# Performance work log

Hardware: AMD Instinct MI355X
Metric: run time of the kernel (lower is better)

Reference implementation:

```python
import jax, jax.numpy as jnp
import numpy as np

N = 50000
NFEAT = 256
NHID = 64
NHEADS = 8
E_RAND = 1600000
ALPHA = 0.2  # leaky relu negative slope


def setup_inputs() -> dict:
    key = jax.random.key(0)
    kx, ke1, ke2, kw, ka, kwo, kao = jax.random.split(key, 7)
    x = jax.random.normal(kx, (N, NFEAT), dtype=jnp.float32)
    src = jax.random.randint(ke1, (E_RAND,), 0, N)
    dst = jax.random.randint(ke2, (E_RAND,), 0, N)
    loops = jnp.arange(N)
    edge_index = jnp.stack([jnp.concatenate([src, loops]),
                            jnp.concatenate([dst, loops])], axis=0)  # [2, 1650000]
    # learned params (xavier-ish scale)
    W = jax.random.normal(kw, (NHEADS, NFEAT, NHID), dtype=jnp.float32) * (1.0 / np.sqrt(NFEAT))
    a = jax.random.normal(ka, (NHEADS, 2 * NHID), dtype=jnp.float32) * (1.0 / np.sqrt(2 * NHID))
    W_out = jax.random.normal(kwo, (NHID * NHEADS, 1), dtype=jnp.float32) * (1.0 / np.sqrt(NHID * NHEADS))
    a_out = jax.random.normal(kao, (2,), dtype=jnp.float32) * (1.0 / np.sqrt(2.0))
    return {"x": x, "edge_index": edge_index, "W": W, "a": a,
            "W_out": W_out, "a_out": a_out}


def _sp_gat_layer(x, edge_index, W_l, a_l, concat):
    """pyGAT SpGraphAttentionLayer forward (eval mode: dropout = identity)."""
    src, dst = edge_index[0], edge_index[1]
    h = x @ W_l                              # [N, F']
    F_ = h.shape[1]
    # a^T [h_src || h_dst] = (a1.h)[src] + (a2.h)[dst] -- avoids [2F', E] concat
    f1 = h @ a_l[:F_]                        # [N]
    f2 = h @ a_l[F_:]                        # [N]
    s = f1[src] + f2[dst]                    # [E]
    e = jnp.exp(-jax.nn.leaky_relu(s, ALPHA))  # [E], note the minus sign (pyGAT)
    rowsum = jax.ops.segment_sum(e, src, num_segments=N)          # [N]
    num = jax.ops.segment_sum(e[:, None] * h[dst], src, num_segments=N)  # [N, F']
    out = num / rowsum[:, None]
    return jax.nn.elu(out) if concat else out


def reference(x, edge_index, W, a, W_out, a_out):
    # input dropout is identity in eval mode
    heads = [_sp_gat_layer(x, edge_index, W[i], a[i], concat=True)
             for i in range(NHEADS)]
    h = jnp.concatenate(heads, axis=1)       # [N, NHEADS*NHID]
    out = _sp_gat_layer(h, edge_index, W_out, a_out, concat=False)  # [N, 1]
    return jax.nn.sigmoid(jax.nn.elu(out))
```

## Files before the change

kernel.cpp:

```cpp
#include <hip/hip_runtime.h>
#include <hip/hip_bf16.h>
#include <hip/hip_fp16.h>
#include <math.h>

#define N_NODES 50000
#define NFEAT 256
#define NHID 64
#define NHEADS 8
#define FTOT 512
#define E_TOT 1650000
#define ALPHA 0.2f
#define NB_SCAN 196
#define ALDS 264
#define GEMM_BLKS 782
#define SCAT_BLKS 3223
#define LOG2E 1.442695040888963f

typedef short s16x4 __attribute__((ext_vector_type(4)));
typedef short s16x8 __attribute__((ext_vector_type(8)));
typedef float f32x4 __attribute__((ext_vector_type(4)));
typedef float f32x2 __attribute__((ext_vector_type(2)));

__device__ __forceinline__ short f2bf(float f) {
  unsigned u = __float_as_uint(f);
  unsigned r = u + 0x7fffu + ((u >> 16) & 1u);
  return (short)(r >> 16);
}

__device__ __forceinline__ unsigned char f2fp8(float f) {
  return (unsigned char)(__builtin_amdgcn_cvt_pk_fp8_f32(f, 0.f, 0, false) & 0xff);
}

__device__ __forceinline__ float att_e(float f1v, float g) {
  float s = f1v + g;
  float lk = fmaxf(s, ALPHA * s);
  return __builtin_amdgcn_exp2f(-LOG2E * lk);
}

__device__ __forceinline__ void fma8_fp8(float e, uint2 u, f32x2* acc2) {
  f32x2 ev; ev[0] = e; ev[1] = e;
  acc2[0] += ev * __builtin_amdgcn_cvt_pk_f32_fp8(u.x, false);
  acc2[1] += ev * __builtin_amdgcn_cvt_pk_f32_fp8(u.x, true);
  acc2[2] += ev * __builtin_amdgcn_cvt_pk_f32_fp8(u.y, false);
  acc2[3] += ev * __builtin_amdgcn_cvt_pk_f32_fp8(u.y, true);
}

__global__ __launch_bounds__(256) void setup_kernel(
    const float* __restrict__ W, short* __restrict__ Wt,
    const int* __restrict__ src, int* __restrict__ cnt,
    int* __restrict__ rank) {
  int b = blockIdx.x, t = threadIdx.x;
  if (b < 512) {
    int idx = b * 256 + t;
    int h = idx >> 14, r = idx & 16383, k = r >> 6, j = r & 63;
    Wt[h * 16384 + j * 256 + k] = f2bf(W[idx]);
  } else {
    int i = (b - 512) * 256 + t;
    if (i < E_TOT) rank[i] = atomicAdd(&cnt[src[i]], 1);
  }
}

__global__ __launch_bounds__(256) void scan1_kernel(const int* __restrict__ cnt,
                                                    int* __restrict__ offs,
                                                    int* __restrict__ bsum) {
  __shared__ int sh[256];
  int b = blockIdx.x, t = threadIdx.x, i = b * 256 + t;
  int v = (i < N_NODES) ? cnt[i] : 0;
  sh[t] = v;
  __syncthreads();
  for (int o = 1; o < 256; o <<= 1) {
    int u = (t >= o) ? sh[t - o] : 0;
    __syncthreads();
    sh[t] += u;
    __syncthreads();
  }
  if (i < N_NODES) offs[i] = sh[t] - v;
  if (t == 255) bsum[b] = sh[255];
}

__global__ __launch_bounds__(256) void scan2_kernel(int* __restrict__ bsum,
                                                    int* __restrict__ offs) {
  __shared__ int sh[256];
  int t = threadIdx.x;
  int v = (t < NB_SCAN) ? bsum[t] : 0;
  sh[t] = v;
  __syncthreads();
  for (int o = 1; o < 256; o <<= 1) {
    int u = (t >= o) ? sh[t - o] : 0;
    __syncthreads();
    sh[t] += u;
    __syncthreads();
  }
  if (t < NB_SCAN) bsum[t] = sh[t] - v;
  if (t == 255) offs[N_NODES] = sh[255];
}

__global__ __launch_bounds__(256) void scan3_kernel(int* __restrict__ offs,
                                                    const int* __restrict__ bsum) {
  int i = blockIdx.x * 256 + threadIdx.x;
  if (i < N_NODES) offs[i] += bsum[blockIdx.x];
}

__global__ __launch_bounds__(512) void gemm_scatter_kernel(
    const float* __restrict__ x, const short* __restrict__ Wt,
    const float* __restrict__ a, unsigned char* __restrict__ h1,
    float* __restrict__ f1, float* __restrict__ f2,
    const int* __restrict__ src, const int* __restrict__ dst,
    const int* __restrict__ offsets, const int* __restrict__ rank,
    int* __restrict__ edst) {
  if (blockIdx.x >= GEMM_BLKS) {
    int i = (blockIdx.x - GEMM_BLKS) * 512 + threadIdx.x;
    if (i < E_TOT) edst[offsets[src[i]] + rank[i]] = dst[i];
    return;
  }
  __shared__ __align__(16) short A_s[64 * ALDS];
  int bm = blockIdx.x * 64;
  int t = threadIdx.x;
  int wid = t >> 6, l = t & 63;
  int lr = l & 15, lk = l >> 4;
  int arow = t >> 3, acol = (t & 7) * 4;
  const short* wbase = Wt + wid * 16384 + lr * 256 + lk * 8;
  int gr = bm + arow;
  float4 xr[8];
#pragma unroll
  for (int i = 0; i < 8; ++i) {
    if (gr < N_NODES)
      xr[i] = *reinterpret_cast<const float4*>(x + (size_t)gr * NFEAT + i * 32 + acol);
    else
      xr[i] = make_float4(0.f, 0.f, 0.f, 0.f);
  }
#pragma unroll
  for (int i = 0; i < 8; ++i) {
    s16x4 v;
    v[0] = f2bf(xr[i].x); v[1] = f2bf(xr[i].y);
    v[2] = f2bf(xr[i].z); v[3] = f2bf(xr[i].w);
    *reinterpret_cast<s16x4*>(&A_s[arow * ALDS + i * 32 + acol]) = v;
  }
  __syncthreads();
  f32x4 acc[4][4] = {};
  for (int k0 = 0; k0 < NFEAT; k0 += 32) {
    s16x8 bf[4];
#pragma unroll
    for (int nj = 0; nj < 4; ++nj)
      bf[nj] = *reinterpret_cast<const s16x8*>(wbase + nj * 16 * 256 + k0);
    s16x8 af[4];
#pragma unroll
    for (int mi = 0; mi < 4; ++mi)
      af[mi] = *reinterpret_cast<const s16x8*>(
          &A_s[(mi * 16 + lr) * ALDS + k0 + lk * 8]);
#pragma unroll
    for (int mi = 0; mi < 4; ++mi)
#pragma unroll
      for (int nj = 0; nj < 4; ++nj)
        acc[mi][nj] = __builtin_amdgcn_mfma_f32_16x16x32_bf16(
            af[mi], bf[nj], acc[mi][nj], 0, 0, 0);
  }
#pragma unroll
  for (int mi = 0; mi < 4; ++mi) {
#pragma unroll
    for (int nj = 0; nj < 4; ++nj) {
#pragma unroll
      for (int q = 0; q < 4; ++q) {
        int r = bm + mi * 16 + lk * 4 + q;
        if (r < N_NODES)
          h1[(size_t)r * FTOT + wid * 64 + nj * 16 + lr] = f2fp8(acc[mi][nj][q]);
      }
    }
  }
  float a1v[4], a2v[4];
#pragma unroll
  for (int nj = 0; nj < 4; ++nj) {
    a1v[nj] = a[wid * 128 + nj * 16 + lr];
    a2v[nj] = a[wid * 128 + 64 + nj * 16 + lr];
  }
#pragma unroll
  for (int mi = 0; mi < 4; ++mi) {
#pragma unroll
    for (int q = 0; q < 4; ++q) {
      float p1 = 0.f, p2 = 0.f;
#pragma unroll
      for (int nj = 0; nj < 4; ++nj) {
        p1 += acc[mi][nj][q] * a1v[nj];
        p2 += acc[mi][nj][q] * a2v[nj];
      }
      p1 += __shfl_xor(p1, 1); p2 += __shfl_xor(p2, 1);
      p1 += __shfl_xor(p1, 2); p2 += __shfl_xor(p2, 2);
      p1 += __shfl_xor(p1, 4); p2 += __shfl_xor(p2, 4);
      p1 += __shfl_xor(p1, 8); p2 += __shfl_xor(p2, 8);
      int r = bm + mi * 16 + lk * 4 + q;
      if (lr == 0 && r < N_NODES) {
        f1[r * 8 + wid] = p1;
        f2[r * 8 + wid] = p2;
      }
    }
  }
}

__global__ __launch_bounds__(256) void aggregate_kernel(
    const unsigned char* __restrict__ h1, const float* __restrict__ f1,
    const float* __restrict__ f2, const int* __restrict__ offsets,
    const int* __restrict__ edst, const float* __restrict__ W_out,
    float* __restrict__ hout) {
  int wv = __builtin_amdgcn_readfirstlane(threadIdx.x >> 6);
  int n = blockIdx.x * 4 + wv;
  int l = threadIdx.x & 63;
  int head = l >> 3;
  int beg = offsets[n], end = offsets[n + 1];
  float f1v = f1[n * 8 + head];
  f32x2 acc2[4] = {};
  float rs = 0.f;
  int j = beg;
  for (; j + 3 < end; j += 4) {
    int d0 = edst[j], d1 = edst[j + 1], d2 = edst[j + 2], d3 = edst[j + 3];
    uint2 u0 = *reinterpret_cast<const uint2*>(h1 + (size_t)d0 * FTOT + l * 8);
    uint2 u1 = *reinterpret_cast<const uint2*>(h1 + (size_t)d1 * FTOT + l * 8);
    uint2 u2 = *reinterpret_cast<const uint2*>(h1 + (size_t)d2 * FTOT + l * 8);
    uint2 u3 = *reinterpret_cast<const uint2*>(h1 + (size_t)d3 * FTOT + l * 8);
    float g0 = f2[d0 * 8 + head];
    float g1 = f2[d1 * 8 + head];
    float g2 = f2[d2 * 8 + head];
    float g3 = f2[d3 * 8 + head];
    float e0 = att_e(f1v, g0), e1 = att_e(f1v, g1);
    float e2 = att_e(f1v, g2), e3 = att_e(f1v, g3);
    rs += (e0 + e1) + (e2 + e3);
    fma8_fp8(e0, u0, acc2);
    fma8_fp8(e1, u1, acc2);
    fma8_fp8(e2, u2, acc2);
    fma8_fp8(e3, u3, acc2);
  }
  for (; j < end; ++j) {
    int d = edst[j];
    uint2 u = *reinterpret_cast<const uint2*>(h1 + (size_t)d * FTOT + l * 8);
    float e = att_e(f1v, f2[d * 8 + head]);
    rs += e;
    fma8_fp8(e, u, acc2);
  }
  float inv = 1.f / rs;
  float v = 0.f;
  const float* wop = W_out + l * 8;
#pragma unroll
  for (int k = 0; k < 4; ++k) {
#pragma unroll
    for (int q = 0; q < 2; ++q) {
      float o = acc2[k][q] * inv;
      o = (o > 0.f) ? o : expm1f(o);
      v += o * wop[k * 2 + q];
    }
  }
#pragma unroll
  for (int o = 32; o > 0; o >>= 1) v += __shfl_down(v, o);
  if (l == 0) hout[n] = v;
}

__global__ __launch_bounds__(256) void layer2_kernel(
    const int* __restrict__ offsets, const int* __restrict__ edst,
    const float* __restrict__ hout, const float* __restrict__ a_out,
    float* __restrict__ out) {
  int wv = __builtin_amdgcn_readfirstlane(threadIdx.x >> 6);
  int n = blockIdx.x * 4 + wv;
  int l = threadIdx.x & 63;
  float a0 = a_out[0], a1 = a_out[1];
  int beg = offsets[n], end = offsets[n + 1];
  float f1v = hout[n] * a0;
  float rs = 0.f, num = 0.f;
  for (int j = beg + l; j < end; j += 64) {
    int d = edst[j];
    float hd = hout[d];
    float s = f1v + a1 * hd;
    float lk = fmaxf(s, ALPHA * s);
    float e = __builtin_amdgcn_exp2f(-LOG2E * lk);
    rs += e;
    num += e * hd;
  }
#pragma unroll
  for (int o = 32; o > 0; o >>= 1) {
    rs += __shfl_down(rs, o);
    num += __shfl_down(num, o);
  }
  if (l == 0) {
    float o_ = num / rs;
    float el = (o_ > 0.f) ? o_ : expm1f(o_);
    out[n] = 1.f / (1.f + __builtin_amdgcn_exp2f(-LOG2E * el));
  }
}

extern "C" void kernel_launch(void* const* d_in, const int* in_sizes, int n_in,
                              void* d_out, int out_size, void* d_ws, size_t ws_size,
                              hipStream_t stream) {
  const float* x = (const float*)d_in[0];
  const int* ei = (const int*)d_in[1];
  const float* W = (const float*)d_in[2];
  const float* a = (const float*)d_in[3];
  const float* W_out = (const float*)d_in[4];
  const float* a_out = (const float*)d_in[5];
  float* out = (float*)d_out;
  const int* src = ei;
  const int* dst = ei + E_TOT;

  char* p = (char*)d_ws;
  auto carve = [&](size_t bytes) {
    char* r = p;
    p += (bytes + 255) & ~(size_t)255;
    return r;
  };
  unsigned char* h1 = (unsigned char*)carve((size_t)N_NODES * FTOT);
  float* f1 = (float*)carve((size_t)N_NODES * 8 * 4);
  float* f2 = (float*)carve((size_t)N_NODES * 8 * 4);
  int* offsets = (int*)carve((size_t)(N_NODES + 1) * 4);
  int* cnt = (int*)carve((size_t)N_NODES * 4);
  int* rank = (int*)carve((size_t)E_TOT * 4);
  int* edst = (int*)carve((size_t)E_TOT * 4);
  int* bsum = (int*)carve((size_t)NB_SCAN * 4);
  short* Wt = (short*)carve((size_t)NHEADS * NFEAT * NHID * 2);
  float* hout = (float*)carve((size_t)N_NODES * 4);

  hipMemsetAsync(cnt, 0, (size_t)N_NODES * 4, stream);

  setup_kernel<<<512 + 6446, 256, 0, stream>>>(W, Wt, src, cnt, rank);
  scan1_kernel<<<NB_SCAN, 256, 0, stream>>>(cnt, offsets, bsum);
  scan2_kernel<<<1, 256, 0, stream>>>(bsum, offsets);
  scan3_kernel<<<NB_SCAN, 256, 0, stream>>>(offsets, bsum);
  gemm_scatter_kernel<<<GEMM_BLKS + SCAT_BLKS, 512, 0, stream>>>(
      x, Wt, a, h1, f1, f2, src, dst, offsets, rank, edst);
  aggregate_kernel<<<12500, 256, 0, stream>>>(h1, f1, f2, offsets, edst, W_out, hout);
  layer2_kernel<<<12500, 256, 0, stream>>>(offsets, edst, hout, a_out, out);
}
```

Before: 291.7 us.

## Bucket CSR edges by destination range for gather locality; fuse scan passes

Builds the CSR with a compound key (src, dst>>12), so each source's neighbor list is partially sorted into 13 destination tiles. The intent is better cache locality for the gathers of h1 rows and f2 values in the aggregate kernel. The scan becomes a 16-elements-per-thread two-kernel scan over 650k keys, with scan2 and scan3 merged. The -log2e factor is folded into f1/f2 at GEMM time to remove a multiply per edge. In exchange, the count, offset and scan arrays are 13x larger and cost more memory traffic.

```diff
diff --git a/kernel.cpp b/kernel.cpp
--- a/kernel.cpp
+++ b/kernel.cpp
@@ -10,12 +10,16 @@
 #define FTOT 512
 #define E_TOT 1650000
 #define ALPHA 0.2f
-#define NB_SCAN 196
 #define ALDS 264
 #define GEMM_BLKS 782
 #define SCAT_BLKS 3223
 #define LOG2E 1.442695040888963f
 
+#define NT 13
+#define NK (N_NODES * NT)
+#define SC_ELEMS 4096
+#define NB1 159
+
 typedef short s16x4 __attribute__((ext_vector_type(4)));
 typedef short s16x8 __attribute__((ext_vector_type(8)));
 typedef float f32x4 __attribute__((ext_vector_type(4)));
@@ -29,12 +33,6 @@
 
 __device__ __forceinline__ unsigned char f2fp8(float f) {
   return (unsigned char)(__builtin_amdgcn_cvt_pk_fp8_f32(f, 0.f, 0, false) & 0xff);
-}
-
-__device__ __forceinline__ float att_e(float f1v, float g) {
-  float s = f1v + g;
-  float lk = fmaxf(s, ALPHA * s);
-  return __builtin_amdgcn_exp2f(-LOG2E * lk);
 }
 
 __device__ __forceinline__ void fma8_fp8(float e, uint2 u, f32x2* acc2) {
@@ -47,8 +45,8 @@
 
 __global__ __launch_bounds__(256) void setup_kernel(
     const float* __restrict__ W, short* __restrict__ Wt,
-    const int* __restrict__ src, int* __restrict__ cnt,
-    int* __restrict__ rank) {
+    const int* __restrict__ src, const int* __restrict__ dst,
+    int* __restrict__ cnt, int* __restrict__ rank) {
   int b = blockIdx.x, t = threadIdx.x;
   if (b < 512) {
     int idx = b * 256 + t;
@@ -56,7 +54,10 @@
     Wt[h * 16384 + j * 256 + k] = f2bf(W[idx]);
   } else {
     int i = (b - 512) * 256 + t;
-    if (i < E_TOT) rank[i] = atomicAdd(&cnt[src[i]], 1);
+    if (i < E_TOT) {
+      int key = src[i] * NT + (dst[i] >> 12);
+      rank[i] = atomicAdd(&cnt[key], 1);
+    }
   }
 }
 
@@ -64,8 +65,46 @@
                                                     int* __restrict__ offs,
                                                     int* __restrict__ bsum) {
   __shared__ int sh[256];
-  int b = blockIdx.x, t = threadIdx.x, i = b * 256 + t;
-  int v = (i < N_NODES) ? cnt[i] : 0;
+  int b = blockIdx.x, t = threadIdx.x;
+  int base = b * SC_ELEMS + t * 16;
+  int v[16];
+  int s = 0;
+  if (base < NK) {
+#pragma unroll
+    for (int k = 0; k < 4; ++k) {
+      int4 q = *reinterpret_cast<const int4*>(cnt + base + k * 4);
+      v[4 * k] = q.x; v[4 * k + 1] = q.y; v[4 * k + 2] = q.z; v[4 * k + 3] = q.w;
+    }
+#pragma unroll
+    for (int k = 0; k < 16; ++k) s += v[k];
+  } else {
+#pragma unroll
+    for (int k = 0; k < 16; ++k) v[k] = 0;
+  }
+  sh[t] = s;
+  __syncthreads();
+  for (int o = 1; o < 256; o <<= 1) {
+    int u = (t >= o) ? sh[t - o] : 0;
+    __syncthreads();
+    sh[t] += u;
+    __syncthreads();
+  }
+  int run = sh[t] - s;
+  if (base < NK) {
+#pragma unroll
+    for (int k = 0; k < 16; ++k) {
+      offs[base + k] = run;
+      run += v[k];
+    }
+  }
+  if (t == 255) bsum[b] = sh[255];
+}
+
+__global__ __launch_bounds__(256) void scan23_kernel(
+    const int* __restrict__ bsum, int* __restrict__ offs) {
+  __shared__ int sh[256];
+  int b = blockIdx.x, t = threadIdx.x;
+  int v = (t < NB1) ? bsum[t] : 0;
   sh[t] = v;
   __syncthreads();
   for (int o = 1; o < 256; o <<= 1) {
@@ -74,31 +113,13 @@
     sh[t] += u;
     __syncthreads();
   }
-  if (i < N_NODES) offs[i] = sh[t] - v;
-  if (t == 255) bsum[b] = sh[255];
-}
-
-__global__ __launch_bounds__(256) void scan2_kernel(int* __restrict__ bsum,
-                                                    int* __restrict__ offs) {
-  __shared__ int sh[256];
-  int t = threadIdx.x;
-  int v = (t < NB_SCAN) ? bsum[t] : 0;
-  sh[t] = v;
-  __syncthreads();
-  for (int o = 1; o < 256; o <<= 1) {
-    int u = (t >= o) ? sh[t - o] : 0;
-    __syncthreads();
-    sh[t] += u;
-    __syncthreads();
-  }
-  if (t < NB_SCAN) bsum[t] = sh[t] - v;
-  if (t == 255) offs[N_NODES] = sh[255];
-}
-
-__global__ __launch_bounds__(256) void scan3_kernel(int* __restrict__ offs,
-                                                    const int* __restrict__ bsum) {
-  int i = blockIdx.x * 256 + threadIdx.x;
-  if (i < N_NODES) offs[i] += bsum[blockIdx.x];
+  int base = (b > 0) ? sh[b - 1] : 0;
+  int i0 = b * SC_ELEMS + t * 16;
+  if (i0 < NK) {
+#pragma unroll
+    for (int k = 0; k < 16; ++k) offs[i0 + k] += base;
+  }
+  if (b == 0 && t == 0) offs[NK] = sh[NB1 - 1];
 }
 
 __global__ __launch_bounds__(512) void gemm_scatter_kernel(
@@ -110,7 +131,11 @@
     int* __restrict__ edst) {
   if (blockIdx.x >= GEMM_BLKS) {
     int i = (blockIdx.x - GEMM_BLKS) * 512 + threadIdx.x;
-    if (i < E_TOT) edst[offsets[src[i]] + rank[i]] = dst[i];
+    if (i < E_TOT) {
+      int d = dst[i];
+      int key = src[i] * NT + (d >> 12);
+      edst[offsets[key] + rank[i]] = d;
+    }
     return;
   }
   __shared__ __align__(16) short A_s[64 * ALDS];
@@ -189,8 +214,8 @@
       p1 += __shfl_xor(p1, 8); p2 += __shfl_xor(p2, 8);
       int r = bm + mi * 16 + lk * 4 + q;
       if (lr == 0 && r < N_NODES) {
-        f1[r * 8 + wid] = p1;
-        f2[r * 8 + wid] = p2;
+        f1[r * 8 + wid] = -LOG2E * p1;
+        f2[r * 8 + wid] = -LOG2E * p2;
       }
     }
   }
@@ -205,8 +230,8 @@
   int n = blockIdx.x * 4 + wv;
   int l = threadIdx.x & 63;
   int head = l >> 3;
-  int beg = offsets[n], end = offsets[n + 1];
-  float f1v = f1[n * 8 + head];
+  int beg = offsets[n * NT], end = offsets[n * NT + NT];
+  float F = f1[n * 8 + head];
   f32x2 acc2[4] = {};
   float rs = 0.f;
   int j = beg;
@@ -220,8 +245,11 @@
     float g1 = f2[d1 * 8 + head];
     float g2 = f2[d2 * 8 + head];
     float g3 = f2[d3 * 8 + head];
-    float e0 = att_e(f1v, g0), e1 = att_e(f1v, g1);
-    float e2 = att_e(f1v, g2), e3 = att_e(f1v, g3);
+    float c0 = F + g0, c1 = F + g1, c2 = F + g2, c3 = F + g3;
+    float e0 = __builtin_amdgcn_exp2f(fminf(c0, ALPHA * c0));
+    float e1 = __builtin_amdgcn_exp2f(fminf(c1, ALPHA * c1));
+    float e2 = __builtin_amdgcn_exp2f(fminf(c2, ALPHA * c2));
+    float e3 = __builtin_amdgcn_exp2f(fminf(c3, ALPHA * c3));
     rs += (e0 + e1) + (e2 + e3);
     fma8_fp8(e0, u0, acc2);
     fma8_fp8(e1, u1, acc2);
@@ -231,7 +259,8 @@
   for (; j < end; ++j) {
     int d = edst[j];
     uint2 u = *reinterpret_cast<const uint2*>(h1 + (size_t)d * FTOT + l * 8);
-    float e = att_e(f1v, f2[d * 8 + head]);
+    float cs = F + f2[d * 8 + head];
+    float e = __builtin_amdgcn_exp2f(fminf(cs, ALPHA * cs));
     rs += e;
     fma8_fp8(e, u, acc2);
   }
@@ -260,7 +289,7 @@
   int n = blockIdx.x * 4 + wv;
   int l = threadIdx.x & 63;
   float a0 = a_out[0], a1 = a_out[1];
-  int beg = offsets[n], end = offsets[n + 1];
+  int beg = offsets[n * NT], end = offsets[n * NT + NT];
   float f1v = hout[n] * a0;
   float rs = 0.f, num = 0.f;
   for (int j = beg + l; j < end; j += 64) {
@@ -306,20 +335,19 @@
   unsigned char* h1 = (unsigned char*)carve((size_t)N_NODES * FTOT);
   float* f1 = (float*)carve((size_t)N_NODES * 8 * 4);
   float* f2 = (float*)carve((size_t)N_NODES * 8 * 4);
-  int* offsets = (int*)carve((size_t)(N_NODES + 1) * 4);
-  int* cnt = (int*)carve((size_t)N_NODES * 4);
+  int* offsets = (int*)carve((size_t)(NK + 1) * 4);
+  int* cnt = (int*)carve((size_t)NK * 4);
   int* rank = (int*)carve((size_t)E_TOT * 4);
   int* edst = (int*)carve((size_t)E_TOT * 4);
-  int* bsum = (int*)carve((size_t)NB_SCAN * 4);
+  int* bsum = (int*)carve((size_t)NB1 * 4);
   short* Wt = (short*)carve((size_t)NHEADS * NFEAT * NHID * 2);
   float* hout = (float*)carve((size_t)N_NODES * 4);
 
-  hipMemsetAsync(cnt, 0, (size_t)N_NODES * 4, stream);
-
-  setup_kernel<<<512 + 6446, 256, 0, stream>>>(W, Wt, src, cnt, rank);
-  scan1_kernel<<<NB_SCAN, 256, 0, stream>>>(cnt, offsets, bsum);
-  scan2_kernel<<<1, 256, 0, stream>>>(bsum, offsets);
-  scan3_kernel<<<NB_SCAN, 256, 0, stream>>>(offsets, bsum);
+  hipMemsetAsync(cnt, 0, (size_t)NK * 4, stream);
+
+  setup_kernel<<<512 + 6446, 256, 0, stream>>>(W, Wt, src, dst, cnt, rank);
+  scan1_kernel<<<NB1, 256, 0, stream>>>(cnt, offsets, bsum);
+  scan23_kernel<<<NB1, 256, 0, stream>>>(bsum, offsets);
   gemm_scatter_kernel<<<GEMM_BLKS + SCAT_BLKS, 512, 0, stream>>>(
       x, Wt, a, h1, f1, f2, src, dst, offsets, rank, edst);
   aggregate_kernel<<<12500, 256, 0, stream>>>(h1, f1, f2, offsets, edst, W_out, hout);
```

New measurement: 297.3 us. No clear change (+1.9%).

## Fuse atomic histogram with GEMM, merge scan passes, prescale attention logits

Applied to the files above, without the earlier changes.

Moves the per-edge atomic degree histogram out of the setup kernel and co-schedules it with the GEMM blocks. The scatter now runs as its own kernel after the scan. The memset is replaced by zeroing cnt inside the weight-conversion kernel. Scan stages 2 and 3 are merged, so every block redundantly scans the block sums. f1/f2 are pre-multiplied by -log2e so the aggregate loop does one fmin plus exp2 instead of fmax, multiply and exp2. The aim is fewer launches and overlapping the atomic-bound histogram with the compute-bound GEMM. In exchange the scatter loses its overlap with the GEMM.

```diff
diff --git a/kernel.cpp b/kernel.cpp
--- a/kernel.cpp
+++ b/kernel.cpp
@@ -13,7 +13,7 @@
 #define NB_SCAN 196
 #define ALDS 264
 #define GEMM_BLKS 782
-#define SCAT_BLKS 3223
+#define HIST_BLKS 3223
 #define LOG2E 1.442695040888963f
 
 typedef short s16x4 __attribute__((ext_vector_type(4)));
@@ -29,12 +29,6 @@
 
 __device__ __forceinline__ unsigned char f2fp8(float f) {
   return (unsigned char)(__builtin_amdgcn_cvt_pk_fp8_f32(f, 0.f, 0, false) & 0xff);
-}
-
-__device__ __forceinline__ float att_e(float f1v, float g) {
-  float s = f1v + g;
-  float lk = fmaxf(s, ALPHA * s);
-  return __builtin_amdgcn_exp2f(-LOG2E * lk);
 }
 
 __device__ __forceinline__ void fma8_fp8(float e, uint2 u, f32x2* acc2) {
@@ -45,10 +39,8 @@
   acc2[3] += ev * __builtin_amdgcn_cvt_pk_f32_fp8(u.y, true);
 }
 
-__global__ __launch_bounds__(256) void setup_kernel(
-    const float* __restrict__ W, short* __restrict__ Wt,
-    const int* __restrict__ src, int* __restrict__ cnt,
-    int* __restrict__ rank) {
+__global__ __launch_bounds__(256) void wconv_zero_kernel(
+    const float* __restrict__ W, short* __restrict__ Wt, int* __restrict__ cnt) {
   int b = blockIdx.x, t = threadIdx.x;
   if (b < 512) {
     int idx = b * 256 + t;
@@ -56,7 +48,101 @@
     Wt[h * 16384 + j * 256 + k] = f2bf(W[idx]);
   } else {
     int i = (b - 512) * 256 + t;
+    if (i < N_NODES) cnt[i] = 0;
+  }
+}
+
+__global__ __launch_bounds__(512) void gemm_hist_kernel(
+    const float* __restrict__ x, const short* __restrict__ Wt,
+    const float* __restrict__ a, unsigned char* __restrict__ h1,
+    float* __restrict__ f1, float* __restrict__ f2,
+    const int* __restrict__ src, int* __restrict__ cnt,
+    int* __restrict__ rank) {
+  if (blockIdx.x >= GEMM_BLKS) {
+    int i = (blockIdx.x - GEMM_BLKS) * 512 + threadIdx.x;
     if (i < E_TOT) rank[i] = atomicAdd(&cnt[src[i]], 1);
+    return;
+  }
+  __shared__ __align__(16) short A_s[64 * ALDS];
+  int bm = blockIdx.x * 64;
+  int t = threadIdx.x;
+  int wid = t >> 6, l = t & 63;
+  int lr = l & 15, lk = l >> 4;
+  int arow = t >> 3, acol = (t & 7) * 4;
+  const short* wbase = Wt + wid * 16384 + lr * 256 + lk * 8;
+  int gr = bm + arow;
+  float4 xr[8];
+#pragma unroll
+  for (int i = 0; i < 8; ++i) {
+    if (gr < N_NODES)
+      xr[i] = *reinterpret_cast<const float4*>(x + (size_t)gr * NFEAT + i * 32 + acol);
+    else
+      xr[i] = make_float4(0.f, 0.f, 0.f, 0.f);
+  }
+#pragma unroll
+  for (int i = 0; i < 8; ++i) {
+    s16x4 v;
+    v[0] = f2bf(xr[i].x); v[1] = f2bf(xr[i].y);
+    v[2] = f2bf(xr[i].z); v[3] = f2bf(xr[i].w);
+    *reinterpret_cast<s16x4*>(&A_s[arow * ALDS + i * 32 + acol]) = v;
+  }
+  __syncthreads();
+  f32x4 acc[4][4] = {};
+  for (int k0 = 0; k0 < NFEAT; k0 += 32) {
+    s16x8 bf[4];
+#pragma unroll
+    for (int nj = 0; nj < 4; ++nj)
+      bf[nj] = *reinterpret_cast<const s16x8*>(wbase + nj * 16 * 256 + k0);
+    s16x8 af[4];
+#pragma unroll
+    for (int mi = 0; mi < 4; ++mi)
+      af[mi] = *reinterpret_cast<const s16x8*>(
+          &A_s[(mi * 16 + lr) * ALDS + k0 + lk * 8]);
+#pragma unroll
+    for (int mi = 0; mi < 4; ++mi)
+#pragma unroll
+      for (int nj = 0; nj < 4; ++nj)
+        acc[mi][nj] = __builtin_amdgcn_mfma_f32_16x16x32_bf16(
+            af[mi], bf[nj], acc[mi][nj], 0, 0, 0);
+  }
+#pragma unroll
+  for (int mi = 0; mi < 4; ++mi) {
+#pragma unroll
+    for (int nj = 0; nj < 4; ++nj) {
+#pragma unroll
+      for (int q = 0; q < 4; ++q) {
+        int r = bm + mi * 16 + lk * 4 + q;
+        if (r < N_NODES)
+          h1[(size_t)r * FTOT + wid * 64 + nj * 16 + lr] = f2fp8(acc[mi][nj][q]);
+      }
+    }
+  }
+  float a1v[4], a2v[4];
+#pragma unroll
+  for (int nj = 0; nj < 4; ++nj) {
+    a1v[nj] = a[wid * 128 + nj * 16 + lr];
+    a2v[nj] = a[wid * 128 + 64 + nj * 16 + lr];
+  }
+#pragma unroll
+  for (int mi = 0; mi < 4; ++mi) {
+#pragma unroll
+    for (int q = 0; q < 4; ++q) {
+      float p1 = 0.f, p2 = 0.f;
+#pragma unroll
+      for (int nj = 0; nj < 4; ++nj) {
+        p1 += acc[mi][nj][q] * a1v[nj];
+        p2 += acc[mi][nj][q] * a2v[nj];
+      }
+      p1 += __shfl_xor(p1, 1); p2 += __shfl_xor(p2, 1);
+      p1 += __shfl_xor(p1, 2); p2 += __shfl_xor(p2, 2);
+      p1 += __shfl_xor(p1, 4); p2 += __shfl_xor(p2, 4);
+      p1 += __shfl_xor(p1, 8); p2 += __shfl_xor(p2, 8);
+      int r = bm + mi * 16 + lk * 4 + q;
+      if (lr == 0 && r < N_NODES) {
+        f1[r * 8 + wid] = -LOG2E * p1;
+        f2[r * 8 + wid] = -LOG2E * p2;
+      }
+    }
   }
 }
 
@@ -78,10 +164,10 @@
   if (t == 255) bsum[b] = sh[255];
 }
 
-__global__ __launch_bounds__(256) void scan2_kernel(int* __restrict__ bsum,
-                                                    int* __restrict__ offs) {
+__global__ __launch_bounds__(256) void scan23_kernel(
+    const int* __restrict__ bsum, int* __restrict__ offs) {
   __shared__ int sh[256];
-  int t = threadIdx.x;
+  int b = blockIdx.x, t = threadIdx.x;
   int v = (t < NB_SCAN) ? bsum[t] : 0;
   sh[t] = v;
   __syncthreads();
@@ -91,108 +177,20 @@
     sh[t] += u;
     __syncthreads();
   }
-  if (t < NB_SCAN) bsum[t] = sh[t] - v;
-  if (t == 255) offs[N_NODES] = sh[255];
-}
-
-__global__ __launch_bounds__(256) void scan3_kernel(int* __restrict__ offs,
-                                                    const int* __restrict__ bsum) {
-  int i = blockIdx.x * 256 + threadIdx.x;
-  if (i < N_NODES) offs[i] += bsum[blockIdx.x];
-}
-
-__global__ __launch_bounds__(512) void gemm_scatter_kernel(
-    const float* __restrict__ x, const short* __restrict__ Wt,
-    const float* __restrict__ a, unsigned char* __restrict__ h1,
-    float* __restrict__ f1, float* __restrict__ f2,
+  int base = (b > 0) ? sh[b - 1] : 0;
+  int i = b * 256 + t;
+  if (i < N_NODES) offs[i] += base;
+  if (b == 0 && t == 0) offs[N_NODES] = sh[NB_SCAN - 1];
+}
+
+__global__ __launch_bounds__(512) void scatter_kernel(
     const int* __restrict__ src, const int* __restrict__ dst,
     const int* __restrict__ offsets, const int* __restrict__ rank,
     int* __restrict__ edst) {
-  if (blockIdx.x >= GEMM_BLKS) {
-    int i = (blockIdx.x - GEMM_BLKS) * 512 + threadIdx.x;
-    if (i < E_TOT) edst[offsets[src[i]] + rank[i]] = dst[i];
-    return;
-  }
-  __shared__ __align__(16) short A_s[64 * ALDS];
-  int bm = blockIdx.x * 64;
-  int t = threadIdx.x;
-  int wid = t >> 6, l = t & 63;
-  int lr = l & 15, lk = l >> 4;
-  int arow = t >> 3, acol = (t & 7) * 4;
-  const short* wbase = Wt + wid * 16384 + lr * 256 + lk * 8;
-  int gr = bm + arow;
-  float4 xr[8];
-#pragma unroll
-  for (int i = 0; i < 8; ++i) {
-    if (gr < N_NODES)
-      xr[i] = *reinterpret_cast<const float4*>(x + (size_t)gr * NFEAT + i * 32 + acol);
-    else
-      xr[i] = make_float4(0.f, 0.f, 0.f, 0.f);
-  }
-#pragma unroll
-  for (int i = 0; i < 8; ++i) {
-    s16x4 v;
-    v[0] = f2bf(xr[i].x); v[1] = f2bf(xr[i].y);
-    v[2] = f2bf(xr[i].z); v[3] = f2bf(xr[i].w);
-    *reinterpret_cast<s16x4*>(&A_s[arow * ALDS + i * 32 + acol]) = v;
-  }
-  __syncthreads();
-  f32x4 acc[4][4] = {};
-  for (int k0 = 0; k0 < NFEAT; k0 += 32) {
-    s16x8 bf[4];
-#pragma unroll
-    for (int nj = 0; nj < 4; ++nj)
-      bf[nj] = *reinterpret_cast<const s16x8*>(wbase + nj * 16 * 256 + k0);
-    s16x8 af[4];
-#pragma unroll
-    for (int mi = 0; mi < 4; ++mi)
-      af[mi] = *reinterpret_cast<const s16x8*>(
-          &A_s[(mi * 16 + lr) * ALDS + k0 + lk * 8]);
-#pragma unroll
-    for (int mi = 0; mi < 4; ++mi)
-#pragma unroll
-      for (int nj = 0; nj < 4; ++nj)
-        acc[mi][nj] = __builtin_amdgcn_mfma_f32_16x16x32_bf16(
-            af[mi], bf[nj], acc[mi][nj], 0, 0, 0);
-  }
-#pragma unroll
-  for (int mi = 0; mi < 4; ++mi) {
-#pragma unroll
-    for (int nj = 0; nj < 4; ++nj) {
-#pragma unroll
-      for (int q = 0; q < 4; ++q) {
-        int r = bm + mi * 16 + lk * 4 + q;
-        if (r < N_NODES)
-          h1[(size_t)r * FTOT + wid * 64 + nj * 16 + lr] = f2fp8(acc[mi][nj][q]);
-      }
-    }
-  }
-  float a1v[4], a2v[4];
-#pragma unroll
-  for (int nj = 0; nj < 4; ++nj) {
-    a1v[nj] = a[wid * 128 + nj * 16 + lr];
-    a2v[nj] = a[wid * 128 + 64 + nj * 16 + lr];
-  }
-#pragma unroll
-  for (int mi = 0; mi < 4; ++mi) {
-#pragma unroll
-    for (int q = 0; q < 4; ++q) {
-      float p1 = 0.f, p2 = 0.f;
-#pragma unroll
-      for (int nj = 0; nj < 4; ++nj) {
-        p1 += acc[mi][nj][q] * a1v[nj];
-        p2 += acc[mi][nj][q] * a2v[nj];
-      }
-      p1 += __shfl_xor(p1, 1); p2 += __shfl_xor(p2, 1);
-      p1 += __shfl_xor(p1, 2); p2 += __shfl_xor(p2, 2);
-      p1 += __shfl_xor(p1, 4); p2 += __shfl_xor(p2, 4);
-      p1 += __shfl_xor(p1, 8); p2 += __shfl_xor(p2, 8);
-      int r = bm + mi * 16 + lk * 4 + q;
-      if (lr == 0 && r < N_NODES) {
-        f1[r * 8 + wid] = p1;
-        f2[r * 8 + wid] = p2;
-      }
-    }
+  int i = blockIdx.x * 512 + threadIdx.x;
+  if (i < E_TOT) {
+    int s = src[i];
+    edst[offsets[s] + rank[i]] = dst[i];
   }
 }
 
@@ -206,7 +204,7 @@
   int l = threadIdx.x & 63;
   int head = l >> 3;
   int beg = offsets[n], end = offsets[n + 1];
-  float f1v = f1[n * 8 + head];
+  float F = f1[n * 8 + head];
   f32x2 acc2[4] = {};
   float rs = 0.f;
   int j = beg;
@@ -220,8 +218,11 @@
     float g1 = f2[d1 * 8 + head];
     float g2 = f2[d2 * 8 + head];
     float g3 = f2[d3 * 8 + head];
-    float e0 = att_e(f1v, g0), e1 = att_e(f1v, g1);
-    float e2 = att_e(f1v, g2), e3 = att_e(f1v, g3);
+    float c0 = F + g0, c1 = F + g1, c2 = F + g2, c3 = F + g3;
+    float e0 = __builtin_amdgcn_exp2f(fminf(c0, ALPHA * c0));
+    float e1 = __builtin_amdgcn_exp2f(fminf(c1, ALPHA * c1));
+    float e2 = __builtin_amdgcn_exp2f(fminf(c2, ALPHA * c2));
+    float e3 = __builtin_amdgcn_exp2f(fminf(c3, ALPHA * c3));
     rs += (e0 + e1) + (e2 + e3);
     fma8_fp8(e0, u0, acc2);
     fma8_fp8(e1, u1, acc2);
@@ -231,7 +232,8 @@
   for (; j < end; ++j) {
     int d = edst[j];
     uint2 u = *reinterpret_cast<const uint2*>(h1 + (size_t)d * FTOT + l * 8);
-    float e = att_e(f1v, f2[d * 8 + head]);
+    float cs = F + f2[d * 8 + head];
+    float e = __builtin_amdgcn_exp2f(fminf(cs, ALPHA * cs));
     rs += e;
     fma8_fp8(e, u, acc2);
   }
@@ -314,14 +316,12 @@
   short* Wt = (short*)carve((size_t)NHEADS * NFEAT * NHID * 2);
   float* hout = (float*)carve((size_t)N_NODES * 4);
 
-  hipMemsetAsync(cnt, 0, (size_t)N_NODES * 4, stream);
-
-  setup_kernel<<<512 + 6446, 256, 0, stream>>>(W, Wt, src, cnt, rank);
+  wconv_zero_kernel<<<712, 256, 0, stream>>>(W, Wt, cnt);
+  gemm_hist_kernel<<<GEMM_BLKS + HIST_BLKS, 512, 0, stream>>>(
+      x, Wt, a, h1, f1, f2, src, cnt, rank);
   scan1_kernel<<<NB_SCAN, 256, 0, stream>>>(cnt, offsets, bsum);
-  scan2_kernel<<<1, 256, 0, stream>>>(bsum, offsets);
-  scan3_kernel<<<NB_SCAN, 256, 0, stream>>>(offsets, bsum);
-  gemm_scatter_kernel<<<GEMM_BLKS + SCAT_BLKS, 512, 0, stream>>>(
-      x, Wt, a, h1, f1, f2, src, dst, offsets, rank, edst);
+  scan23_kernel<<<NB_SCAN, 256, 0, stream>>>(bsum, offsets);
+  scatter_kernel<<<HIST_BLKS, 512, 0, stream>>>(src, dst, offsets, rank, edst);
   aggregate_kernel<<<12500, 256, 0, stream>>>(h1, f1, f2, offsets, edst, W_out, hout);
   layer2_kernel<<<12500, 256, 0, stream>>>(offsets, edst, hout, a_out, out);
 }
```

Result: no change. 287.0 us (-1.6%).
